# Optimization experiments

Hardware: AMD Instinct MI355X
Metric: run time of the kernel (lower is better)

Reference implementation:

```python
import jax, jax.numpy as jnp
import numpy as np

B, L, H, E = 16, 4096, 8, 64
IN_CH, OUT_CH, MODES = 512, 512, 64


def setup_inputs() -> dict:
    key = jax.random.key(0)
    kq, kk, kv, k1, k2 = jax.random.split(key, 5)
    scale = 1.0 / (IN_CH * OUT_CH)
    q = jax.random.normal(kq, (B, L, H, E), jnp.float32)
    k = jax.random.normal(kk, (B, L, H, E), jnp.float32)
    v = jax.random.normal(kv, (B, L, H, E), jnp.float32)
    mask = jnp.zeros((B, L), jnp.bool_)
    # learned params: (heads=8, in_ch//8, out_ch//8, modes), torch.rand init * scale
    w1 = scale * jax.random.uniform(k1, (8, IN_CH // 8, OUT_CH // 8, MODES), jnp.float32)
    w2 = scale * jax.random.uniform(k2, (8, IN_CH // 8, OUT_CH // 8, MODES), jnp.float32)
    return {"q": q, "k": k, "v": v, "mask": mask, "w1": w1, "w2": w2}


def reference(q, k, v, mask, w1, w2):
    # q: [B, L, H, E]; k, v, mask unused by the original forward.
    Bq, Lq, Hq, Eq = q.shape
    modes = w1.shape[-1]
    x = jnp.transpose(q, (0, 2, 3, 1))          # [B, H, E, L]
    x_ft = jnp.fft.rfft(x, axis=-1)             # [B, H, E, L//2+1] complex64
    # mode_select_method='else' => index = [0..modes-1], wi == i, so the
    # per-mode gather/einsum/scatter loop collapses to a slice + batched einsum.
    sel = x_ft[..., :modes]                     # [B, H, E_in, modes]
    wc = w1 + 1j * w2                           # [H, E_in, E_out, modes] complex
    out_modes = jnp.einsum('bhim,hiom->bhom', sel, wc)  # [B, H, E_out, modes]
    nfreq = Lq // 2 + 1
    out_ft = jnp.zeros((Bq, Hq, w1.shape[2], nfreq), jnp.complex64)
    out_ft = out_ft.at[..., :modes].set(out_modes)
    x_out = jnp.fft.irfft(out_ft, n=Lq, axis=-1)  # [B, H, E_out, L] float32
    return x_out
```

## Files before the change

kernel.cpp:

```cpp
#include <hip/hip_runtime.h>
#include <math.h>

#define NB 16
#define NL 4096
#define NH 8
#define NI 64
#define NO 64
#define NM 64
#define QUARTER 1024
#define STEP 1.5339807878856412e-3f

__device__ __forceinline__ int sk(int p) { return p + (p >> 5); }

__global__ __launch_bounds__(256) void k_fwd(const float* __restrict__ q,
                                             float* __restrict__ partial,
                                             int LCF, int CHUNK) {
  const int lc = blockIdx.x, h = blockIdx.y, b = blockIdx.z;
  const int t = threadIdx.x;
  __shared__ float ct[4096];
  __shared__ float4 prep[16][64];

  for (int idx = t; idx < 4096; idx += 256) ct[idx] = cosf((float)idx * STEP);

  const int ig = t & 15;
  const int m0 = (t >> 4) << 2;
  float ar[4][4], ai[4][4];
#pragma unroll
  for (int k = 0; k < 4; ++k)
#pragma unroll
    for (int j = 0; j < 4; ++j) { ar[k][j] = 0.f; ai[k][j] = 0.f; }

  const int lstart = lc * CHUNK;

  for (int tt = 0; tt < CHUNK; tt += 16) {
    __syncthreads();
    {
      const int iA = t & 63;
#pragma unroll
      for (int c = 0; c < 4; ++c) {
        const int lloc = (t >> 6) + (c << 2);
        const int labs = lstart + tt + lloc;
        const float* qp = q + (((size_t)b * NL + labs) * NH + h) * NI + iA;
        const float q0 = qp[0];
        const float q1 = qp[(size_t)QUARTER * NH * NI];
        const float q2 = qp[(size_t)2 * QUARTER * NH * NI];
        const float q3 = qp[(size_t)3 * QUARTER * NH * NI];
        const float E = q0 + q2, F = q1 + q3;
        prep[lloc][iA] = make_float4(E + F, E - F, q0 - q2, q1 - q3);
      }
    }
    __syncthreads();
#pragma unroll 2
    for (int ll = 0; ll < 16; ++ll) {
      const int la = lstart + tt + ll;
      const int p0 = (m0 * la) & 4095;
      const int p1 = (p0 + la) & 4095;
      const int p2 = (p1 + la) & 4095;
      const int p3 = (p2 + la) & 4095;
      const float c0 = ct[p0], s0 = ct[(p0 + 3072) & 4095];
      const float c1 = ct[p1], s1 = ct[(p1 + 3072) & 4095];
      const float c2 = ct[p2], s2 = ct[(p2 + 3072) & 4095];
      const float c3 = ct[p3], s3 = ct[(p3 + 3072) & 4095];
#pragma unroll
      for (int j = 0; j < 4; ++j) {
        const float4 f = prep[ll][ig + (j << 4)];
        ar[0][j] = fmaf(f.x, c0, ar[0][j]);
        ai[0][j] = fmaf(-f.x, s0, ai[0][j]);
        ar[1][j] = fmaf(f.z, c1, ar[1][j]);
        ar[1][j] = fmaf(-f.w, s1, ar[1][j]);
        ai[1][j] = fmaf(-f.z, s1, ai[1][j]);
        ai[1][j] = fmaf(-f.w, c1, ai[1][j]);
        ar[2][j] = fmaf(f.y, c2, ar[2][j]);
        ai[2][j] = fmaf(-f.y, s2, ai[2][j]);
        ar[3][j] = fmaf(f.z, c3, ar[3][j]);
        ar[3][j] = fmaf(f.w, s3, ar[3][j]);
        ai[3][j] = fmaf(f.w, c3, ai[3][j]);
        ai[3][j] = fmaf(-f.z, s3, ai[3][j]);
      }
    }
  }
  float2* dst = (float2*)partial + (((size_t)b * NH + h) * LCF + lc) * (NM * NI);
#pragma unroll
  for (int k = 0; k < 4; ++k)
#pragma unroll
    for (int j = 0; j < 4; ++j)
      dst[(m0 + k) * NI + (ig + (j << 4))] = make_float2(ar[k][j], ai[k][j]);
}

__global__ __launch_bounds__(256) void k_mix(const float* __restrict__ partial,
                                             const float* __restrict__ w1,
                                             const float* __restrict__ w2,
                                             float* __restrict__ out2, int LCF) {
  const int og = blockIdx.x, h = blockIdx.y, b = blockIdx.z;
  const int t = threadIdx.x;
  __shared__ float sel_s[2][64][65];

  const float* src = partial + ((size_t)b * NH + h) * LCF * (NM * NI * 2);
  for (int u = t; u < NM * NI * 2; u += 256) {
    float v = 0.f;
    for (int lcx = 0; lcx < LCF; ++lcx) v += src[(size_t)lcx * (NM * NI * 2) + u];
    sel_s[u & 1][(u >> 1) & 63][u >> 7] = v;
  }
  __syncthreads();

  const int o = og * 16 + (t >> 4);
  const int mt = t & 15;
  float ar[4] = {0.f, 0.f, 0.f, 0.f}, ai[4] = {0.f, 0.f, 0.f, 0.f};
  for (int i = 0; i < NI; ++i) {
    const float* w1p = w1 + (((size_t)h * NI + i) * NO + o) * NM;
    const float* w2p = w2 + (((size_t)h * NI + i) * NO + o) * NM;
#pragma unroll
    for (int k = 0; k < 4; ++k) {
      const int m = mt + (k << 4);
      const float re = sel_s[0][i][m];
      const float im = sel_s[1][i][m];
      const float a = w1p[m];
      const float bb = w2p[m];
      ar[k] = fmaf(re, a, ar[k]);
      ar[k] = fmaf(-im, bb, ar[k]);
      ai[k] = fmaf(re, bb, ai[k]);
      ai[k] = fmaf(im, a, ai[k]);
    }
  }
  float2* dst = (float2*)out2 + ((size_t)b * NH + h) * (NM * NO);
#pragma unroll
  for (int k = 0; k < 4; ++k)
    dst[(mt + (k << 4)) * NO + o] = make_float2(ar[k], ai[k]);
}

__global__ __launch_bounds__(256) void k_inv(const float* __restrict__ out2,
                                             float* __restrict__ xout) {
  const int lb = blockIdx.x, h = blockIdx.y, b = blockIdx.z;
  const int t = threadIdx.x;
  __shared__ float ct[4224];
  __shared__ float2 oms[NM * NO];

  for (int idx = t; idx < 4096; idx += 256) ct[sk(idx)] = cosf((float)idx * STEP);

  const float* src = out2 + ((size_t)b * NH + h) * (NM * NO * 2);
  float* omsf = (float*)oms;
  for (int u = t; u < NM * NO * 2; u += 256) {
    const int m = u >> 7;
    const float fac = (m == 0 ? 1.0f : 2.0f) * (1.0f / 4096.0f);
    omsf[u] = src[u] * fac;
  }
  __syncthreads();

  const int lg = t & 15;
  const int og = t >> 4;
  const int o0 = og << 2;
  const int l0 = (lb << 5) + (lg << 1);

  float Tr[4][2][4], Ti[4][2][4];
#pragma unroll
  for (int r = 0; r < 4; ++r)
#pragma unroll
    for (int ll = 0; ll < 2; ++ll)
#pragma unroll
      for (int j = 0; j < 4; ++j) { Tr[r][ll][j] = 0.f; Ti[r][ll][j] = 0.f; }

#pragma unroll
  for (int r = 0; r < 4; ++r) {
    int p0 = (r * l0) & 4095;
    int p1 = (r * (l0 + 1)) & 4095;
    const int d0 = (l0 << 2) & 4095;
    const int d1 = ((l0 + 1) << 2) & 4095;
#pragma unroll 2
    for (int m = r; m < NM; m += 4) {
      const float4 ca = ((const float4*)&oms[m * NO + o0])[0];
      const float4 cb = ((const float4*)&oms[m * NO + o0])[1];
      const float cre[4] = {ca.x, ca.z, cb.x, cb.z};
      const float cim[4] = {ca.y, ca.w, cb.y, cb.w};
      const float c_0 = ct[sk(p0)], s_0 = ct[sk((p0 + 3072) & 4095)];
      const float c_1 = ct[sk(p1)], s_1 = ct[sk((p1 + 3072) & 4095)];
      p0 = (p0 + d0) & 4095;
      p1 = (p1 + d1) & 4095;
#pragma unroll
      for (int j = 0; j < 4; ++j) {
        Tr[r][0][j] = fmaf(cre[j], c_0, Tr[r][0][j]);
        Tr[r][0][j] = fmaf(-cim[j], s_0, Tr[r][0][j]);
        Ti[r][0][j] = fmaf(cre[j], s_0, Ti[r][0][j]);
        Ti[r][0][j] = fmaf(cim[j], c_0, Ti[r][0][j]);
        Tr[r][1][j] = fmaf(cre[j], c_1, Tr[r][1][j]);
        Tr[r][1][j] = fmaf(-cim[j], s_1, Tr[r][1][j]);
        Ti[r][1][j] = fmaf(cre[j], s_1, Ti[r][1][j]);
        Ti[r][1][j] = fmaf(cim[j], c_1, Ti[r][1][j]);
      }
    }
  }

  const size_t obase = ((size_t)b * NH + h) * NO * (size_t)NL;
#pragma unroll
  for (int j = 0; j < 4; ++j) {
    float* orow = xout + obase + (size_t)(o0 + j) * NL;
    float v[4][2];
#pragma unroll
    for (int ll = 0; ll < 2; ++ll) {
      const float a  = Tr[0][ll][j] + Tr[2][ll][j];
      const float bb = Tr[1][ll][j] + Tr[3][ll][j];
      const float c  = Tr[0][ll][j] - Tr[2][ll][j];
      const float d  = Ti[1][ll][j] - Ti[3][ll][j];
      v[0][ll] = a + bb;
      v[1][ll] = c - d;
      v[2][ll] = a - bb;
      v[3][ll] = c + d;
    }
#pragma unroll
    for (int p = 0; p < 4; ++p)
      *(float2*)(orow + p * QUARTER + l0) = make_float2(v[p][0], v[p][1]);
  }
}

extern "C" void kernel_launch(void* const* d_in, const int* in_sizes, int n_in,
                              void* d_out, int out_size, void* d_ws, size_t ws_size,
                              hipStream_t stream) {
  const float* q  = (const float*)d_in[0];
  const float* w1 = (const float*)d_in[4];
  const float* w2 = (const float*)d_in[5];
  float* out = (float*)d_out;

  const size_t out2Elems = (size_t)NB * NH * NM * NO * 2;
  int LCF = 1;
  const int cands[4] = {8, 4, 2, 1};
  for (int ci = 0; ci < 4; ++ci) {
    const size_t pe = (size_t)NB * NH * cands[ci] * NM * NI * 2;
    if ((pe + out2Elems) * sizeof(float) <= ws_size) { LCF = cands[ci]; break; }
  }
  const size_t partialElems = (size_t)NB * NH * LCF * NM * NI * 2;
  float* partial = (float*)d_ws;
  float* out2 = partial + partialElems;

  dim3 blk(256);
  k_fwd<<<dim3(LCF, NH, NB), blk, 0, stream>>>(q, partial, LCF, QUARTER / LCF);
  k_mix<<<dim3(4, NH, NB), blk, 0, stream>>>(partial, w1, w2, out2, LCF);
  k_inv<<<dim3(32, NH, NB), blk, 0, stream>>>(out2, out);
}
```

Measured before the change: 521.5 us.

## Compute inverse DFT as split-bf16 MFMA GEMM against precomputed twiddle table

The inverse transform is rewritten as a GEMM. A bf16 hi/lo twiddle matrix [L x 2*modes], built by a new table kernel, is multiplied with the scaled mode coefficients using 32x32x16 bf16 MFMA. A three-product hi/lo split is meant to keep near-fp32 accuracy. This replaces the scalar FMA loop and its quarter-symmetry butterfly. The new kernel also precomputes the cosine table once for k_fwd instead of each block calling cosf. In exchange it adds a kernel launch, about 2MB of twiddle reads from global memory, and extra workspace use that could lower LCF.

```diff
diff --git a/kernel.cpp b/kernel.cpp
--- a/kernel.cpp
+++ b/kernel.cpp
@@ -10,17 +10,38 @@
 #define QUARTER 1024
 #define STEP 1.5339807878856412e-3f
 
-__device__ __forceinline__ int sk(int p) { return p + (p >> 5); }
+using bf16_t = __bf16;
+using bf16x8 = __attribute__((ext_vector_type(8))) __bf16;
+using f32x16 = __attribute__((ext_vector_type(16))) float;
+
+#define LDW 136
+#define TMC 128
+
+__global__ __launch_bounds__(256) void k_tab(float* __restrict__ ctab,
+                                             bf16_t* __restrict__ Thi,
+                                             bf16_t* __restrict__ Tlo) {
+  const int gid = blockIdx.x * 256 + threadIdx.x;
+  const int l = gid >> 7, mc = gid & 127, m = mc >> 1;
+  const int p = (m * l) & 4095;
+  const float c = cosf((float)p * STEP);
+  const float s = cosf((float)((p + 3072) & 4095) * STEP);
+  const float val = (mc & 1) ? -s : c;
+  const bf16_t hi = (bf16_t)val;
+  Thi[gid] = hi;
+  Tlo[gid] = (bf16_t)(val - (float)hi);
+  if (gid < 4096) ctab[gid] = cosf((float)gid * STEP);
+}
 
 __global__ __launch_bounds__(256) void k_fwd(const float* __restrict__ q,
                                              float* __restrict__ partial,
+                                             const float* __restrict__ ctab,
                                              int LCF, int CHUNK) {
   const int lc = blockIdx.x, h = blockIdx.y, b = blockIdx.z;
   const int t = threadIdx.x;
   __shared__ float ct[4096];
   __shared__ float4 prep[16][64];
 
-  for (int idx = t; idx < 4096; idx += 256) ct[idx] = cosf((float)idx * STEP);
+  for (int idx = t; idx < 4096; idx += 256) ct[idx] = ctab[idx];
 
   const int ig = t & 15;
   const int m0 = (t >> 4) << 2;
@@ -129,86 +150,70 @@
 }
 
 __global__ __launch_bounds__(256) void k_inv(const float* __restrict__ out2,
+                                             const bf16_t* __restrict__ Thi,
+                                             const bf16_t* __restrict__ Tlo,
                                              float* __restrict__ xout) {
   const int lb = blockIdx.x, h = blockIdx.y, b = blockIdx.z;
   const int t = threadIdx.x;
-  __shared__ float ct[4224];
-  __shared__ float2 oms[NM * NO];
-
-  for (int idx = t; idx < 4096; idx += 256) ct[sk(idx)] = cosf((float)idx * STEP);
-
-  const float* src = out2 + ((size_t)b * NH + h) * (NM * NO * 2);
-  float* omsf = (float*)oms;
-  for (int u = t; u < NM * NO * 2; u += 256) {
-    const int m = u >> 7;
-    const float fac = (m == 0 ? 1.0f : 2.0f) * (1.0f / 4096.0f);
-    omsf[u] = src[u] * fac;
+  __shared__ bf16_t Whi[64 * LDW];
+  __shared__ bf16_t Wlo[64 * LDW];
+
+  {
+    const float2* src = (const float2*)out2 + ((size_t)b * NH + h) * (NM * NO);
+    for (int u = t; u < NM * NO; u += 256) {
+      const int m = u >> 6, o = u & 63;
+      const float fac = (m == 0 ? 1.0f : 2.0f) * (1.0f / 4096.0f);
+      const float2 cc = src[u];
+      const float re = cc.x * fac, im = cc.y * fac;
+      const bf16_t reh = (bf16_t)re, imh = (bf16_t)im;
+      Whi[o * LDW + 2 * m] = reh;
+      Whi[o * LDW + 2 * m + 1] = imh;
+      Wlo[o * LDW + 2 * m] = (bf16_t)(re - (float)reh);
+      Wlo[o * LDW + 2 * m + 1] = (bf16_t)(im - (float)imh);
+    }
   }
   __syncthreads();
 
-  const int lg = t & 15;
-  const int og = t >> 4;
-  const int o0 = og << 2;
-  const int l0 = (lb << 5) + (lg << 1);
-
-  float Tr[4][2][4], Ti[4][2][4];
-#pragma unroll
-  for (int r = 0; r < 4; ++r)
-#pragma unroll
-    for (int ll = 0; ll < 2; ++ll)
-#pragma unroll
-      for (int j = 0; j < 4; ++j) { Tr[r][ll][j] = 0.f; Ti[r][ll][j] = 0.f; }
-
-#pragma unroll
-  for (int r = 0; r < 4; ++r) {
-    int p0 = (r * l0) & 4095;
-    int p1 = (r * (l0 + 1)) & 4095;
-    const int d0 = (l0 << 2) & 4095;
-    const int d1 = ((l0 + 1) << 2) & 4095;
-#pragma unroll 2
-    for (int m = r; m < NM; m += 4) {
-      const float4 ca = ((const float4*)&oms[m * NO + o0])[0];
-      const float4 cb = ((const float4*)&oms[m * NO + o0])[1];
-      const float cre[4] = {ca.x, ca.z, cb.x, cb.z};
-      const float cim[4] = {ca.y, ca.w, cb.y, cb.w};
-      const float c_0 = ct[sk(p0)], s_0 = ct[sk((p0 + 3072) & 4095)];
-      const float c_1 = ct[sk(p1)], s_1 = ct[sk((p1 + 3072) & 4095)];
-      p0 = (p0 + d0) & 4095;
-      p1 = (p1 + d1) & 4095;
-#pragma unroll
-      for (int j = 0; j < 4; ++j) {
-        Tr[r][0][j] = fmaf(cre[j], c_0, Tr[r][0][j]);
-        Tr[r][0][j] = fmaf(-cim[j], s_0, Tr[r][0][j]);
-        Ti[r][0][j] = fmaf(cre[j], s_0, Ti[r][0][j]);
-        Ti[r][0][j] = fmaf(cim[j], c_0, Ti[r][0][j]);
-        Tr[r][1][j] = fmaf(cre[j], c_1, Tr[r][1][j]);
-        Tr[r][1][j] = fmaf(-cim[j], s_1, Tr[r][1][j]);
-        Ti[r][1][j] = fmaf(cre[j], s_1, Ti[r][1][j]);
-        Ti[r][1][j] = fmaf(cim[j], c_1, Ti[r][1][j]);
+  const int w = t >> 6, lane = t & 63;
+  const int lrow = lane & 31;
+  const int kh = (lane >> 5) << 3;
+  const int lwave = (lb << 8) + (w << 6);
+
+  f32x16 acc[2][2] = {};
+
+#pragma unroll
+  for (int ks = 0; ks < 8; ++ks) {
+    const int kb = ks * 16 + kh;
+    const bf16x8 ah0 = *(const bf16x8*)&Whi[lrow * LDW + kb];
+    const bf16x8 ah1 = *(const bf16x8*)&Whi[(lrow + 32) * LDW + kb];
+    const bf16x8 al0 = *(const bf16x8*)&Wlo[lrow * LDW + kb];
+    const bf16x8 al1 = *(const bf16x8*)&Wlo[(lrow + 32) * LDW + kb];
+    const size_t r0 = (size_t)(lwave + lrow) * TMC + kb;
+    const size_t r1 = (size_t)(lwave + 32 + lrow) * TMC + kb;
+    const bf16x8 bh0 = *(const bf16x8*)&Thi[r0];
+    const bf16x8 bh1 = *(const bf16x8*)&Thi[r1];
+    const bf16x8 bl0 = *(const bf16x8*)&Tlo[r0];
+    const bf16x8 bl1 = *(const bf16x8*)&Tlo[r1];
+#define MM(a, bb, c) c = __builtin_amdgcn_mfma_f32_32x32x16_bf16(a, bb, c, 0, 0, 0)
+    MM(ah0, bh0, acc[0][0]); MM(ah0, bl0, acc[0][0]); MM(al0, bh0, acc[0][0]);
+    MM(ah0, bh1, acc[0][1]); MM(ah0, bl1, acc[0][1]); MM(al0, bh1, acc[0][1]);
+    MM(ah1, bh0, acc[1][0]); MM(ah1, bl0, acc[1][0]); MM(al1, bh0, acc[1][0]);
+    MM(ah1, bh1, acc[1][1]); MM(ah1, bl1, acc[1][1]); MM(al1, bh1, acc[1][1]);
+#undef MM
+  }
+
+  float* obase = xout + ((size_t)b * NH + h) * NO * (size_t)NL;
+#pragma unroll
+  for (int of = 0; of < 2; ++of)
+#pragma unroll
+    for (int lf = 0; lf < 2; ++lf) {
+      const int lg = lwave + lf * 32 + lrow;
+#pragma unroll
+      for (int r = 0; r < 16; ++r) {
+        const int o = of * 32 + (r & 3) + 8 * (r >> 2) + 4 * (lane >> 5);
+        obase[(size_t)o * NL + lg] = acc[of][lf][r];
       }
     }
-  }
-
-  const size_t obase = ((size_t)b * NH + h) * NO * (size_t)NL;
-#pragma unroll
-  for (int j = 0; j < 4; ++j) {
-    float* orow = xout + obase + (size_t)(o0 + j) * NL;
-    float v[4][2];
-#pragma unroll
-    for (int ll = 0; ll < 2; ++ll) {
-      const float a  = Tr[0][ll][j] + Tr[2][ll][j];
-      const float bb = Tr[1][ll][j] + Tr[3][ll][j];
-      const float c  = Tr[0][ll][j] - Tr[2][ll][j];
-      const float d  = Ti[1][ll][j] - Ti[3][ll][j];
-      v[0][ll] = a + bb;
-      v[1][ll] = c - d;
-      v[2][ll] = a - bb;
-      v[3][ll] = c + d;
-    }
-#pragma unroll
-    for (int p = 0; p < 4; ++p)
-      *(float2*)(orow + p * QUARTER + l0) = make_float2(v[p][0], v[p][1]);
-  }
 }
 
 extern "C" void kernel_launch(void* const* d_in, const int* in_sizes, int n_in,
@@ -220,18 +225,24 @@
   float* out = (float*)d_out;
 
   const size_t out2Elems = (size_t)NB * NH * NM * NO * 2;
+  const size_t tElems = (size_t)NL * TMC;
+  const size_t tabFloats = 4096 + (2 * tElems * sizeof(bf16_t)) / sizeof(float);
   int LCF = 1;
   const int cands[4] = {8, 4, 2, 1};
   for (int ci = 0; ci < 4; ++ci) {
     const size_t pe = (size_t)NB * NH * cands[ci] * NM * NI * 2;
-    if ((pe + out2Elems) * sizeof(float) <= ws_size) { LCF = cands[ci]; break; }
+    if ((pe + out2Elems + tabFloats) * sizeof(float) <= ws_size) { LCF = cands[ci]; break; }
   }
   const size_t partialElems = (size_t)NB * NH * LCF * NM * NI * 2;
   float* partial = (float*)d_ws;
   float* out2 = partial + partialElems;
+  float* ctab = out2 + out2Elems;
+  bf16_t* Thi = (bf16_t*)(ctab + 4096);
+  bf16_t* Tlo = Thi + tElems;
 
   dim3 blk(256);
-  k_fwd<<<dim3(LCF, NH, NB), blk, 0, stream>>>(q, partial, LCF, QUARTER / LCF);
+  k_tab<<<dim3((unsigned)(tElems / 256)), blk, 0, stream>>>(ctab, Thi, Tlo);
+  k_fwd<<<dim3(LCF, NH, NB), blk, 0, stream>>>(q, partial, ctab, LCF, QUARTER / LCF);
   k_mix<<<dim3(4, NH, NB), blk, 0, stream>>>(partial, w1, w2, out2, LCF);
-  k_inv<<<dim3(32, NH, NB), blk, 0, stream>>>(out2, out);
-}
+  k_inv<<<dim3(16, NH, NB), blk, 0, stream>>>(out2, Thi, Tlo, out);
+}
```

Result: faster. 496.5 us (-4.8%).
